# Optimization experiments

Measured on AMD Instinct MI355X. Metric: run time of the kernel, lower is better.

The kernel has to match this reference:

```python
import jax, jax.numpy as jnp
import numpy as np

HEADS = 16
DIM_HEAD = 64
LN_EPS = 1e-3  # keras LayerNormalization default


def setup_inputs() -> dict:
    key = jax.random.key(0)
    ks = jax.random.split(key, 4)
    B, N, D = 8, 512, 1024
    inner = HEADS * DIM_HEAD  # 1024
    return {
        "x": jax.random.normal(ks[0], (B, N, D), dtype=jnp.float32),
        "w_qkv": jax.random.normal(ks[1], (D, 3 * inner), dtype=jnp.float32) * (D ** -0.5),
        "reattn_w": jax.random.normal(ks[2], (HEADS, HEADS), dtype=jnp.float32),
        "ln_gamma": jnp.ones((HEADS,), dtype=jnp.float32),
        "ln_beta": jnp.zeros((HEADS,), dtype=jnp.float32),
        "w_out": jax.random.normal(ks[3], (inner, D), dtype=jnp.float32) * (inner ** -0.5),
        "b_out": jnp.zeros((D,), dtype=jnp.float32),
    }


def reference(x, w_qkv, reattn_w, ln_gamma, ln_beta, w_out, b_out):
    B, N, D = x.shape
    H, dh = HEADS, DIM_HEAD
    scale = dh ** -0.5

    qkv = x @ w_qkv  # [B, N, 3*H*dh]
    q, k, v = jnp.split(qkv, 3, axis=-1)
    # b n (h d) -> b h n d
    to_heads = lambda t: t.reshape(B, N, H, dh).transpose(0, 2, 1, 3)
    q, k, v = to_heads(q), to_heads(k), to_heads(v)

    dots = jnp.einsum("bhid,bhjd->bhij", q, k) * scale  # [B, H, N, N]
    attn = jax.nn.softmax(dots, axis=-1)

    # re-attention: mix across heads
    attn = jnp.einsum("bhij,hg->bgij", attn, reattn_w)

    # LayerNorm over the head axis (axis=1), keras default eps
    mean = jnp.mean(attn, axis=1, keepdims=True)
    var = jnp.var(attn, axis=1, keepdims=True)
    attn = (attn - mean) * jax.lax.rsqrt(var + LN_EPS)
    attn = attn * ln_gamma[None, :, None, None] + ln_beta[None, :, None, None]

    out = jnp.einsum("bhij,bhjd->bhid", attn, v)  # [B, H, N, dh]
    out = out.transpose(0, 2, 1, 3).reshape(B, N, H * dh)  # b h n d -> b n (h d)
    return out @ w_out + b_out
```

## Files before the change

### kernel.cpp

```cpp
#include <hip/hip_runtime.h>
#include <math.h>

#define BB 8
#define NN 512
#define DD 1024
#define HH 16
#define DH 64
#define INNER 1024
#define QKV3 3072
#define PSTR (NN * NN + 64)

typedef __attribute__((ext_vector_type(8))) short short8;
typedef __attribute__((ext_vector_type(4))) float f32x4;

#define AS1 __attribute__((address_space(1)))
#define AS3 __attribute__((address_space(3)))

__device__ __forceinline__ float4 ld4(const float* p) { return *(const float4*)p; }

__device__ __forceinline__ unsigned short f2bf(float f) {
    unsigned u = __float_as_uint(f);
    return (unsigned short)((u + 0x7fffu + ((u >> 16) & 1u)) >> 16);
}
__device__ __forceinline__ float bf2f(unsigned short u) {
    return __uint_as_float(((unsigned)u) << 16);
}

__global__ void conv_bf16(const float* __restrict__ in, unsigned short* __restrict__ out) {
    size_t i = ((size_t)blockIdx.x * 256 + threadIdx.x) * 4;
    float4 v = ld4(in + i);
    ushort4 o;
    o.x = f2bf(v.x); o.y = f2bf(v.y); o.z = f2bf(v.z); o.w = f2bf(v.w);
    *(ushort4*)(out + i) = o;
}

__global__ void convT_bf16(const float* __restrict__ in, unsigned short* __restrict__ out,
                           int K, int N) {
    __shared__ float t[32][33];
    const int n0 = blockIdx.x * 32, k0 = blockIdx.y * 32;
    const int tx = threadIdx.x & 31, ty = threadIdx.x >> 5;
#pragma unroll
    for (int l = 0; l < 4; ++l)
        t[ty + 8 * l][tx] = in[(size_t)(k0 + ty + 8 * l) * N + n0 + tx];
    __syncthreads();
#pragma unroll
    for (int l = 0; l < 4; ++l)
        out[(size_t)(n0 + ty + 8 * l) * K + k0 + tx] = f2bf(t[tx][ty + 8 * l]);
}

__global__ __launch_bounds__(256) void gemm_bf16(
    const unsigned short* __restrict__ A, const unsigned short* __restrict__ Bt,
    float* __restrict__ C, const float* __restrict__ bias, int M, int N, int K) {
    __shared__ short As[128 * 32];
    __shared__ short Bs[128 * 32];
    const int tid = threadIdx.x;
    const int w = tid >> 6, l = tid & 63;
    const int bm = blockIdx.y * 128, bn = blockIdx.x * 128;
    const int wm = (w >> 1) * 64, wn = (w & 1) * 64;
    const int lrow = l & 15, lq = l >> 4;

    f32x4 acc[4][4];
#pragma unroll
    for (int i = 0; i < 4; ++i)
#pragma unroll
        for (int j = 0; j < 4; ++j) acc[i][j] = (f32x4){0.f, 0.f, 0.f, 0.f};

    for (int k0 = 0; k0 < K; k0 += 32) {
#pragma unroll
        for (int t = 0; t < 2; ++t) {
            const int q = w * 2 + t;
            const int li = q * 512 + l * 8;
            const int row = li >> 5, kc = li & 31;
            const unsigned short* ga = A + (size_t)(bm + row) * K + k0 + kc;
            __builtin_amdgcn_global_load_lds(
                (const AS1 void*)ga, (AS3 void*)(As + q * 512), 16, 0, 0);
            const unsigned short* gb = Bt + (size_t)(bn + row) * K + k0 + kc;
            __builtin_amdgcn_global_load_lds(
                (const AS1 void*)gb, (AS3 void*)(Bs + q * 512), 16, 0, 0);
        }
        __syncthreads();

        short8 a[4], b[4];
#pragma unroll
        for (int i = 0; i < 4; ++i)
            a[i] = *(const short8*)(As + (wm + i * 16 + lrow) * 32 + lq * 8);
#pragma unroll
        for (int j = 0; j < 4; ++j)
            b[j] = *(const short8*)(Bs + (wn + j * 16 + lrow) * 32 + lq * 8);
#pragma unroll
        for (int i = 0; i < 4; ++i)
#pragma unroll
            for (int j = 0; j < 4; ++j)
                acc[i][j] = __builtin_amdgcn_mfma_f32_16x16x32_bf16(a[i], b[j], acc[i][j], 0, 0, 0);
        __syncthreads();
    }

#pragma unroll
    for (int i = 0; i < 4; ++i)
#pragma unroll
        for (int j = 0; j < 4; ++j) {
            const int col = bn + wn + j * 16 + lrow;
            const float bv = bias ? bias[col] : 0.f;
#pragma unroll
            for (int r = 0; r < 4; ++r) {
                const int row = bm + wm + i * 16 + lq * 4 + r;
                C[(size_t)row * N + col] = acc[i][j][r] + bv;
            }
        }
}

__device__ __forceinline__ void stage_st(const unsigned short* __restrict__ G, int K,
                                         int row0, int kt, short* dst_half,
                                         int w, int l) {
    const int grow = row0 + w * 16 + (l >> 2);
    const int gcol = kt * 32 + (((l & 3) * 8) ^ ((l & 32) ? 16 : 0));
    __builtin_amdgcn_global_load_lds(
        (const AS1 void*)(G + (size_t)grow * K + gcol),
        (AS3 void*)(dst_half + w * 512), 16, 0, 0);
}

__global__ __launch_bounds__(512, 2) void gemm256_bf(
    const unsigned short* __restrict__ A, const unsigned short* __restrict__ Bt,
    unsigned short* __restrict__ C, int M, int N, int K) {
    __shared__ __align__(16) short lds_[2 * 16384];
    const int tid = threadIdx.x;
    const int w = tid >> 6, l = tid & 63;
    const int wm = w >> 2, wn = w & 3;
    const int lrow = l & 15, lq = l >> 4;
    const int bm = blockIdx.y * 256, bn = blockIdx.x * 256;
    const int NT = K >> 5;

    const int aoff = lrow * 32 + ((lq * 8) ^ ((lrow & 8) ? 16 : 0));
    const int bsub = (wn & 1) * 4;

    f32x4 acc[8][4];
#pragma unroll
    for (int i = 0; i < 8; ++i)
#pragma unroll
        for (int j = 0; j < 4; ++j) acc[i][j] = (f32x4){0.f, 0.f, 0.f, 0.f};

    stage_st(A,  K, bm,       0, lds_ + 0,     w, l);
    stage_st(A,  K, bm + 128, 0, lds_ + 4096,  w, l);
    stage_st(Bt, K, bn,       0, lds_ + 8192,  w, l);
    stage_st(Bt, K, bn + 128, 0, lds_ + 12288, w, l);
    asm volatile("s_waitcnt vmcnt(0)" ::: "memory");
    __builtin_amdgcn_s_barrier();

    for (int t = 0; t < NT; ++t) {
        const int s = t & 1;
        if (t + 1 < NT) {
            short* nb = lds_ + (s ^ 1) * 16384;
            stage_st(A,  K, bm,       t + 1, nb,         w, l);
            stage_st(A,  K, bm + 128, t + 1, nb + 4096,  w, l);
            stage_st(Bt, K, bn,       t + 1, nb + 8192,  w, l);
            stage_st(Bt, K, bn + 128, t + 1, nb + 12288, w, l);
        }
        const short* Ah = lds_ + s * 16384 + wm * 4096;
        const short* Bh = lds_ + s * 16384 + 8192 + (wn >> 1) * 4096;
        short8 a[8], bfr[4];
#pragma unroll
        for (int i = 0; i < 8; ++i)
            a[i] = *(const short8*)(Ah + i * 512 + aoff);
#pragma unroll
        for (int j = 0; j < 4; ++j)
            bfr[j] = *(const short8*)(Bh + (bsub + j) * 512 + aoff);

        asm volatile("s_waitcnt lgkmcnt(0)" ::: "memory");
        __builtin_amdgcn_sched_barrier(0);

        __builtin_amdgcn_s_setprio(1);
#pragma unroll
        for (int i = 0; i < 8; ++i)
#pragma unroll
            for (int j = 0; j < 4; ++j)
                acc[i][j] = __builtin_amdgcn_mfma_f32_16x16x32_bf16(a[i], bfr[j], acc[i][j], 0, 0, 0);
        __builtin_amdgcn_s_setprio(0);

        asm volatile("s_waitcnt vmcnt(0)" ::: "memory");
        __builtin_amdgcn_s_barrier();
    }

#pragma unroll
    for (int fr = 0; fr < 8; ++fr)
#pragma unroll
        for (int fc = 0; fc < 4; ++fc) {
            const int col = bn + wn * 64 + fc * 16 + lrow;
#pragma unroll
            for (int r = 0; r < 4; ++r) {
                const int row = bm + wm * 128 + fr * 16 + lq * 4 + r;
                C[(size_t)row * N + col] = f2bf(acc[fr][fc][r]);
            }
        }
}

__global__ __launch_bounds__(256) void scores_stream(
    const unsigned short* __restrict__ qkvb, unsigned short* __restrict__ attnb,
    float* __restrict__ lsum2) {
    __shared__ unsigned short Ks[256 * 64];
    __shared__ unsigned short obuf[4][16][68];
    const int bh = blockIdx.x;
    const int h = bh & 15, b = bh >> 4;
    const int jh = blockIdx.y;
    const int w = threadIdx.x >> 6, l = threadIdx.x & 63;
    const int i0 = blockIdx.z * 64 + w * 16;
    const int lrow = l & 15, lq = l >> 4;

    const unsigned short* kbase =
        qkvb + (size_t)(b * NN + jh * 256) * QKV3 + INNER + h * DH;
#pragma unroll
    for (int i = 0; i < 8; ++i) {
        const int r = (w * 8 + i) * 8 + (l >> 3);
        const int c = (l & 7) ^ (r & 7);
        __builtin_amdgcn_global_load_lds(
            (const AS1 void*)(kbase + (size_t)r * QKV3 + c * 8),
            (AS3 void*)(Ks + (w * 8 + i) * 512), 16, 0, 0);
    }

    const unsigned short* qb = qkvb + (size_t)(b * NN) * QKV3 + h * DH + lq * 8;
    const short8 qf0 = *(const short8*)(qb + (size_t)(i0 + lrow) * QKV3);
    const short8 qf1 = *(const short8*)(qb + (size_t)(i0 + lrow) * QKV3 + 32);

    asm volatile("s_waitcnt vmcnt(0)" ::: "memory");
    __syncthreads();

    unsigned short* obase = attnb + (size_t)bh * PSTR + (size_t)i0 * NN + jh * 256;
    const int sw = lrow & 7;
    float lacc = 0.f;
#pragma unroll
    for (int jt = 0; jt < 16; ++jt) {
        const int R = jt * 16 + lrow;
        const short8 kf0 = *(const short8*)(Ks + R * 64 + ((lq ^ sw) * 8));
        const short8 kf1 = *(const short8*)(Ks + R * 64 + (((4 + lq) ^ sw) * 8));
        f32x4 acc = (f32x4){0.f, 0.f, 0.f, 0.f};
        acc = __builtin_amdgcn_mfma_f32_16x16x32_bf16(kf0, qf0, acc, 0, 0, 0);
        acc = __builtin_amdgcn_mfma_f32_16x16x32_bf16(kf1, qf1, acc, 0, 0, 0);
        float e0 = __expf(acc[0] * 0.125f);
        float e1 = __expf(acc[1] * 0.125f);
        float e2 = __expf(acc[2] * 0.125f);
        float e3 = __expf(acc[3] * 0.125f);
        lacc += (e0 + e1) + (e2 + e3);
        ushort4 o;
        o.x = f2bf(e0); o.y = f2bf(e1); o.z = f2bf(e2); o.w = f2bf(e3);
        *(ushort4*)(&obuf[w][lrow][(jt & 3) * 16 + lq * 4]) = o;
        if ((jt & 3) == 3) {
            const int jb = (jt >> 2) * 64;
#pragma unroll
            for (int q = 0; q < 4; ++q) {
                const int rr = q * 4 + (l >> 4);
                const int cc = l & 15;
                *(ushort4*)(obase + (size_t)rr * NN + jb + cc * 4) =
                    *(const ushort4*)(&obuf[w][rr][cc * 4]);
            }
        }
    }
    lacc += __shfl_xor(lacc, 16, 64);
    lacc += __shfl_xor(lacc, 32, 64);
    if (lq == 0)
        lsum2[(size_t)jh * BB * HH * NN + (size_t)bh * NN + i0 + lrow] = lacc;
}

__global__ void reattn_ln_bf(unsigned short* __restrict__ attnb,
                             const float* __restrict__ lsum2,
                             const float* __restrict__ rw,
                             const float* __restrict__ gamma,
                             const float* __restrict__ beta) {
    __shared__ float w[16][16];
    __shared__ float gs[16], bs[16];
    const int tid = threadIdx.x;
    ((float*)w)[tid] = rw[tid];
    if (tid < 16) { gs[tid] = gamma[tid]; bs[tid] = beta[tid]; }
    __syncthreads();

    const size_t idx = (size_t)blockIdx.x * 256 + tid;
    const int j4 = (int)(idx & 127);
    const int i = (int)((idx >> 7) & 511);
    const int b = (int)(idx >> 16);
    unsigned short* base = attnb + (size_t)(b * HH) * PSTR + (size_t)i * NN + j4 * 4;
    const float* l0 = lsum2 + (size_t)(b * HH) * NN + i;
    const float* l1 = l0 + (size_t)BB * HH * NN;

    float v[16][4];
#pragma unroll
    for (int h = 0; h < 16; ++h) {
        const float linv = 1.0f / (l0[h * NN] + l1[h * NN]);
        ushort4 u = *(const ushort4*)(base + (size_t)h * PSTR);
        v[h][0] = bf2f(u.x) * linv; v[h][1] = bf2f(u.y) * linv;
        v[h][2] = bf2f(u.z) * linv; v[h][3] = bf2f(u.w) * linv;
    }
    float o[16][4];
    float me[4] = {0.f, 0.f, 0.f, 0.f};
#pragma unroll
    for (int g = 0; g < 16; ++g) {
        float s0 = 0.f, s1 = 0.f, s2 = 0.f, s3 = 0.f;
#pragma unroll
        for (int h = 0; h < 16; ++h) {
            const float wg = w[h][g];
            s0 += v[h][0] * wg; s1 += v[h][1] * wg;
            s2 += v[h][2] * wg; s3 += v[h][3] * wg;
        }
        o[g][0] = s0; o[g][1] = s1; o[g][2] = s2; o[g][3] = s3;
        me[0] += s0; me[1] += s1; me[2] += s2; me[3] += s3;
    }
#pragma unroll
    for (int r = 0; r < 4; ++r) me[r] *= 0.0625f;
    float va[4] = {0.f, 0.f, 0.f, 0.f};
#pragma unroll
    for (int g = 0; g < 16; ++g)
#pragma unroll
        for (int r = 0; r < 4; ++r) {
            float d = o[g][r] - me[r];
            va[r] += d * d;
        }
    float ri[4];
#pragma unroll
    for (int r = 0; r < 4; ++r) ri[r] = rsqrtf(va[r] * 0.0625f + 1e-3f);
#pragma unroll
    for (int g = 0; g < 16; ++g) {
        ushort4 u;
        u.x = f2bf((o[g][0] - me[0]) * ri[0] * gs[g] + bs[g]);
        u.y = f2bf((o[g][1] - me[1]) * ri[1] * gs[g] + bs[g]);
        u.z = f2bf((o[g][2] - me[2]) * ri[2] * gs[g] + bs[g]);
        u.w = f2bf((o[g][3] - me[3]) * ri[3] * gs[g] + bs[g]);
        *(ushort4*)(base + (size_t)g * PSTR) = u;
    }
}

__global__ void transpose_v(const unsigned short* __restrict__ qkvb,
                            unsigned short* __restrict__ vT) {
    __shared__ unsigned short t[32][33];
    const int bh = blockIdx.z;
    const int h = bh & 15, b = bh >> 4;
    const int j0 = blockIdx.x * 32, d0 = blockIdx.y * 32;
    const int tx = threadIdx.x & 31, ty = threadIdx.x >> 5;
    const unsigned short* src = qkvb + (size_t)(b * NN) * QKV3 + 2 * INNER + h * DH;
#pragma unroll
    for (int k = 0; k < 4; ++k)
        t[ty + 8 * k][tx] = src[(size_t)(j0 + ty + 8 * k) * QKV3 + d0 + tx];
    __syncthreads();
    unsigned short* dst = vT + (size_t)bh * DH * NN;
#pragma unroll
    for (int k = 0; k < 4; ++k)
        dst[(size_t)(d0 + ty + 8 * k) * NN + j0 + tx] = t[tx][ty + 8 * k];
}

__global__ __launch_bounds__(256) void pv_mfma(
    const unsigned short* __restrict__ attnb, const unsigned short* __restrict__ vT,
    unsigned short* __restrict__ outhb) {
    const int bh = blockIdx.x;
    const int h = bh & 15, b = bh >> 4;
    const int i0 = blockIdx.y * 128;
    __shared__ short Ps[128 * 64];
    __shared__ short Vs[64 * 64];
    const int tid = threadIdx.x;
    const int w = tid >> 6, l = tid & 63;
    const int lrow = l & 15, lq = l >> 4;
    const int lr8 = l >> 3;
    const int swd = ((l & 7) ^ (lr8 & 7)) * 8;

    f32x4 acc[2][4];
#pragma unroll
    for (int ic = 0; ic < 2; ++ic)
#pragma unroll
        for (int dt = 0; dt < 4; ++dt) acc[ic][dt] = (f32x4){0.f, 0.f, 0.f, 0.f};

    const unsigned short* pb = attnb + (size_t)bh * PSTR + (size_t)i0 * NN;
    const unsigned short* vb = vT + (size_t)bh * DH * NN;

    for (int j0 = 0; j0 < NN; j0 += 64) {
#pragma unroll
        for (int t = 0; t < 4; ++t) {
            int c = w * 4 + t;
            int r = c * 8 + lr8;
            __builtin_amdgcn_global_load_lds(
                (const AS1 void*)(pb + (size_t)r * NN + j0 + swd),
                (AS3 void*)(Ps + c * 512), 16, 0, 0);
        }
#pragma unroll
        for (int t = 0; t < 2; ++t) {
            int c = w * 2 + t;
            int d = c * 8 + lr8;
            __builtin_amdgcn_global_load_lds(
                (const AS1 void*)(vb + (size_t)d * NN + j0 + swd),
                (AS3 void*)(Vs + c * 512), 16, 0, 0);
        }
        __syncthreads();

#pragma unroll
        for (int kh = 0; kh < 2; ++kh) {
            short8 vf[4];
#pragma unroll
            for (int dt = 0; dt < 4; ++dt)
                vf[dt] = *(const short8*)(Vs + (dt * 16 + lrow) * 64 + (((kh * 4 + lq) ^ (lrow & 7)) * 8));
#pragma unroll
            for (int ic = 0; ic < 2; ++ic) {
                short8 pf = *(const short8*)(Ps + (w * 32 + ic * 16 + lrow) * 64 + (((kh * 4 + lq) ^ (lrow & 7)) * 8));
#pragma unroll
                for (int dt = 0; dt < 4; ++dt)
                    acc[ic][dt] = __builtin_amdgcn_mfma_f32_16x16x32_bf16(vf[dt], pf, acc[ic][dt], 0, 0, 0);
            }
        }
        __syncthreads();
    }

#pragma unroll
    for (int ic = 0; ic < 2; ++ic) {
        unsigned short* orow = outhb +
            ((size_t)(b * NN + i0 + w * 32 + ic * 16 + lrow)) * INNER + h * DH + lq * 4;
#pragma unroll
        for (int dt = 0; dt < 4; ++dt) {
            ushort4 o;
            o.x = f2bf(acc[ic][dt][0]); o.y = f2bf(acc[ic][dt][1]);
            o.z = f2bf(acc[ic][dt][2]); o.w = f2bf(acc[ic][dt][3]);
            *(ushort4*)(orow + dt * 16) = o;
        }
    }
}

extern "C" void kernel_launch(void* const* d_in, const int* in_sizes, int n_in,
                              void* d_out, int out_size, void* d_ws, size_t ws_size,
                              hipStream_t stream) {
    const float* x        = (const float*)d_in[0];
    const float* w_qkv    = (const float*)d_in[1];
    const float* reattn_w = (const float*)d_in[2];
    const float* ln_gamma = (const float*)d_in[3];
    const float* ln_beta  = (const float*)d_in[4];
    const float* w_out    = (const float*)d_in[5];
    const float* b_out    = (const float*)d_in[6];
    float* out = (float*)d_out;

    unsigned short* qkvb  = (unsigned short*)d_ws;
    unsigned short* attnb = qkvb + (size_t)BB * NN * QKV3;
    unsigned short* vTb   = attnb + (size_t)BB * HH * PSTR;
    unsigned short* outhb = vTb + (size_t)BB * HH * DH * NN;
    unsigned short* xb    = outhb + (size_t)BB * NN * INNER;
    unsigned short* wqkvT = xb + (size_t)BB * NN * DD;
    unsigned short* woutT = wqkvT + (size_t)DD * QKV3;
    float*          lsum2 = (float*)(woutT + (size_t)INNER * INNER);

    dim3 blk(256);

    conv_bf16<<<dim3((BB * NN * DD) / 1024), blk, 0, stream>>>(x, xb);
    convT_bf16<<<dim3(QKV3 / 32, DD / 32), blk, 0, stream>>>(w_qkv, wqkvT, DD, QKV3);
    convT_bf16<<<dim3(INNER / 32, INNER / 32), blk, 0, stream>>>(w_out, woutT, INNER, INNER);

    gemm256_bf<<<dim3(QKV3 / 256, (BB * NN) / 256), dim3(512), 0, stream>>>(
        xb, wqkvT, qkvb, BB * NN, QKV3, DD);

    scores_stream<<<dim3(BB * HH, 2, NN / 64), blk, 0, stream>>>(qkvb, attnb, lsum2);

    reattn_ln_bf<<<dim3((BB * NN * NN) / 1024), blk, 0, stream>>>(
        attnb, lsum2, reattn_w, ln_gamma, ln_beta);

    transpose_v<<<dim3(NN / 32, DH / 32, BB * HH), blk, 0, stream>>>(qkvb, vTb);

    pv_mfma<<<dim3(BB * HH, NN / 128), blk, 0, stream>>>(attnb, vTb, outhb);

    gemm_bf16<<<dim3(INNER / 128, (BB * NN) / 128), blk, 0, stream>>>(
        outhb, woutT, out, b_out, BB * NN, INNER, INNER);
}
```

Before: 219.2 us.

## Double-buffer LDS in output GEMM and PV kernels, fuse conversion launches

```diff
diff --git a/kernel.cpp b/kernel.cpp
--- a/kernel.cpp
+++ b/kernel.cpp
@@ -26,19 +26,31 @@
     return __uint_as_float(((unsigned)u) << 16);
 }
 
-__global__ void conv_bf16(const float* __restrict__ in, unsigned short* __restrict__ out) {
-    size_t i = ((size_t)blockIdx.x * 256 + threadIdx.x) * 4;
-    float4 v = ld4(in + i);
-    ushort4 o;
-    o.x = f2bf(v.x); o.y = f2bf(v.y); o.z = f2bf(v.z); o.w = f2bf(v.w);
-    *(ushort4*)(out + i) = o;
-}
-
-__global__ void convT_bf16(const float* __restrict__ in, unsigned short* __restrict__ out,
-                           int K, int N) {
+__global__ void preprocess(const float* __restrict__ x, unsigned short* __restrict__ xb,
+                           const float* __restrict__ wq, unsigned short* __restrict__ wqT,
+                           const float* __restrict__ wo, unsigned short* __restrict__ woT) {
     __shared__ float t[32][33];
-    const int n0 = blockIdx.x * 32, k0 = blockIdx.y * 32;
-    const int tx = threadIdx.x & 31, ty = threadIdx.x >> 5;
+    const int tid = threadIdx.x;
+    const int bx = blockIdx.x;
+    if (bx < 4096) {
+        size_t i = ((size_t)bx * 256 + tid) * 4;
+        float4 v = ld4(x + i);
+        ushort4 o;
+        o.x = f2bf(v.x); o.y = f2bf(v.y); o.z = f2bf(v.z); o.w = f2bf(v.w);
+        *(ushort4*)(xb + i) = o;
+        return;
+    }
+    const float* in; unsigned short* out; int K, N, n0, k0;
+    if (bx < 7168) {
+        const int bb = bx - 4096;
+        in = wq; out = wqT; K = DD; N = QKV3;
+        n0 = (bb % 96) * 32; k0 = (bb / 96) * 32;
+    } else {
+        const int bb = bx - 7168;
+        in = wo; out = woT; K = INNER; N = INNER;
+        n0 = (bb & 31) * 32; k0 = (bb >> 5) * 32;
+    }
+    const int tx = tid & 31, ty = tid >> 5;
 #pragma unroll
     for (int l = 0; l < 4; ++l)
         t[ty + 8 * l][tx] = in[(size_t)(k0 + ty + 8 * l) * N + n0 + tx];
@@ -48,16 +60,34 @@
         out[(size_t)(n0 + ty + 8 * l) * K + k0 + tx] = f2bf(t[tx][ty + 8 * l]);
 }
 
+__device__ __forceinline__ void stage128(const unsigned short* __restrict__ A,
+                                         const unsigned short* __restrict__ Bt,
+                                         int K, int bm, int bn, int kt,
+                                         short* sb, int w, int l) {
+#pragma unroll
+    for (int t = 0; t < 2; ++t) {
+        const int q = w * 2 + t;
+        const int li = q * 512 + l * 8;
+        const int row = li >> 5, kc = li & 31;
+        __builtin_amdgcn_global_load_lds(
+            (const AS1 void*)(A + (size_t)(bm + row) * K + kt * 32 + kc),
+            (AS3 void*)(sb + q * 512), 16, 0, 0);
+        __builtin_amdgcn_global_load_lds(
+            (const AS1 void*)(Bt + (size_t)(bn + row) * K + kt * 32 + kc),
+            (AS3 void*)(sb + 4096 + q * 512), 16, 0, 0);
+    }
+}
+
 __global__ __launch_bounds__(256) void gemm_bf16(
     const unsigned short* __restrict__ A, const unsigned short* __restrict__ Bt,
     float* __restrict__ C, const float* __restrict__ bias, int M, int N, int K) {
-    __shared__ short As[128 * 32];
-    __shared__ short Bs[128 * 32];
+    __shared__ __align__(16) short lds_[2 * 8192];
     const int tid = threadIdx.x;
     const int w = tid >> 6, l = tid & 63;
     const int bm = blockIdx.y * 128, bn = blockIdx.x * 128;
     const int wm = (w >> 1) * 64, wn = (w & 1) * 64;
     const int lrow = l & 15, lq = l >> 4;
+    const int NT = K >> 5;
 
     f32x4 acc[4][4];
 #pragma unroll
@@ -65,34 +95,37 @@
 #pragma unroll
         for (int j = 0; j < 4; ++j) acc[i][j] = (f32x4){0.f, 0.f, 0.f, 0.f};
 
-    for (int k0 = 0; k0 < K; k0 += 32) {
-#pragma unroll
-        for (int t = 0; t < 2; ++t) {
-            const int q = w * 2 + t;
-            const int li = q * 512 + l * 8;
-            const int row = li >> 5, kc = li & 31;
-            const unsigned short* ga = A + (size_t)(bm + row) * K + k0 + kc;
-            __builtin_amdgcn_global_load_lds(
-                (const AS1 void*)ga, (AS3 void*)(As + q * 512), 16, 0, 0);
-            const unsigned short* gb = Bt + (size_t)(bn + row) * K + k0 + kc;
-            __builtin_amdgcn_global_load_lds(
-                (const AS1 void*)gb, (AS3 void*)(Bs + q * 512), 16, 0, 0);
-        }
-        __syncthreads();
-
+    stage128(A, Bt, K, bm, bn, 0, lds_, w, l);
+    asm volatile("s_waitcnt vmcnt(0)" ::: "memory");
+    __builtin_amdgcn_s_barrier();
+
+    for (int t = 0; t < NT; ++t) {
+        const int s = t & 1;
+        if (t + 1 < NT)
+            stage128(A, Bt, K, bm, bn, t + 1, lds_ + (s ^ 1) * 8192, w, l);
+        const short* As_ = lds_ + s * 8192;
+        const short* Bs_ = As_ + 4096;
         short8 a[4], b[4];
 #pragma unroll
         for (int i = 0; i < 4; ++i)
-            a[i] = *(const short8*)(As + (wm + i * 16 + lrow) * 32 + lq * 8);
+            a[i] = *(const short8*)(As_ + (wm + i * 16 + lrow) * 32 + lq * 8);
 #pragma unroll
         for (int j = 0; j < 4; ++j)
-            b[j] = *(const short8*)(Bs + (wn + j * 16 + lrow) * 32 + lq * 8);
+            b[j] = *(const short8*)(Bs_ + (wn + j * 16 + lrow) * 32 + lq * 8);
+
+        asm volatile("s_waitcnt lgkmcnt(0)" ::: "memory");
+        __builtin_amdgcn_sched_barrier(0);
+
+        __builtin_amdgcn_s_setprio(1);
 #pragma unroll
         for (int i = 0; i < 4; ++i)
 #pragma unroll
             for (int j = 0; j < 4; ++j)
                 acc[i][j] = __builtin_amdgcn_mfma_f32_16x16x32_bf16(a[i], b[j], acc[i][j], 0, 0, 0);
-        __syncthreads();
+        __builtin_amdgcn_s_setprio(0);
+
+        asm volatile("s_waitcnt vmcnt(0)" ::: "memory");
+        __builtin_amdgcn_s_barrier();
     }
 
 #pragma unroll
@@ -343,14 +376,36 @@
         dst[(size_t)(d0 + ty + 8 * k) * NN + j0 + tx] = t[tx][ty + 8 * k];
 }
 
+__device__ __forceinline__ void stage_pv(const unsigned short* __restrict__ pb,
+                                         const unsigned short* __restrict__ vb,
+                                         int j0, short* Ps, short* Vs,
+                                         int w, int l, int lr8, int swd) {
+#pragma unroll
+    for (int t = 0; t < 4; ++t) {
+        int c = w * 4 + t;
+        int r = c * 8 + lr8;
+        __builtin_amdgcn_global_load_lds(
+            (const AS1 void*)(pb + (size_t)r * NN + j0 + swd),
+            (AS3 void*)(Ps + c * 512), 16, 0, 0);
+    }
+#pragma unroll
+    for (int t = 0; t < 2; ++t) {
+        int c = w * 2 + t;
+        int d = c * 8 + lr8;
+        __builtin_amdgcn_global_load_lds(
+            (const AS1 void*)(vb + (size_t)d * NN + j0 + swd),
+            (AS3 void*)(Vs + c * 512), 16, 0, 0);
+    }
+}
+
 __global__ __launch_bounds__(256) void pv_mfma(
     const unsigned short* __restrict__ attnb, const unsigned short* __restrict__ vT,
     unsigned short* __restrict__ outhb) {
     const int bh = blockIdx.x;
     const int h = bh & 15, b = bh >> 4;
     const int i0 = blockIdx.y * 128;
-    __shared__ short Ps[128 * 64];
-    __shared__ short Vs[64 * 64];
+    __shared__ __align__(16) short Ps[2][128 * 64];
+    __shared__ __align__(16) short Vs[2][64 * 64];
     const int tid = threadIdx.x;
     const int w = tid >> 6, l = tid & 63;
     const int lrow = l & 15, lq = l >> 4;
@@ -366,40 +421,44 @@
     const unsigned short* pb = attnb + (size_t)bh * PSTR + (size_t)i0 * NN;
     const unsigned short* vb = vT + (size_t)bh * DH * NN;
 
-    for (int j0 = 0; j0 < NN; j0 += 64) {
-#pragma unroll
-        for (int t = 0; t < 4; ++t) {
-            int c = w * 4 + t;
-            int r = c * 8 + lr8;
-            __builtin_amdgcn_global_load_lds(
-                (const AS1 void*)(pb + (size_t)r * NN + j0 + swd),
-                (AS3 void*)(Ps + c * 512), 16, 0, 0);
-        }
-#pragma unroll
-        for (int t = 0; t < 2; ++t) {
-            int c = w * 2 + t;
-            int d = c * 8 + lr8;
-            __builtin_amdgcn_global_load_lds(
-                (const AS1 void*)(vb + (size_t)d * NN + j0 + swd),
-                (AS3 void*)(Vs + c * 512), 16, 0, 0);
-        }
-        __syncthreads();
-
+    stage_pv(pb, vb, 0, Ps[0], Vs[0], w, l, lr8, swd);
+    asm volatile("s_waitcnt vmcnt(0)" ::: "memory");
+    __builtin_amdgcn_s_barrier();
+
+    for (int js = 0; js < 8; ++js) {
+        const int s = js & 1;
+        if (js + 1 < 8)
+            stage_pv(pb, vb, (js + 1) * 64, Ps[s ^ 1], Vs[s ^ 1], w, l, lr8, swd);
+
+        short8 vf[8], pf[4];
 #pragma unroll
         for (int kh = 0; kh < 2; ++kh) {
-            short8 vf[4];
 #pragma unroll
             for (int dt = 0; dt < 4; ++dt)
-                vf[dt] = *(const short8*)(Vs + (dt * 16 + lrow) * 64 + (((kh * 4 + lq) ^ (lrow & 7)) * 8));
-#pragma unroll
-            for (int ic = 0; ic < 2; ++ic) {
-                short8 pf = *(const short8*)(Ps + (w * 32 + ic * 16 + lrow) * 64 + (((kh * 4 + lq) ^ (lrow & 7)) * 8));
+                vf[kh * 4 + dt] = *(const short8*)(
+                    &Vs[s][(dt * 16 + lrow) * 64 + (((kh * 4 + lq) ^ (lrow & 7)) * 8)]);
+#pragma unroll
+            for (int ic = 0; ic < 2; ++ic)
+                pf[kh * 2 + ic] = *(const short8*)(
+                    &Ps[s][(w * 32 + ic * 16 + lrow) * 64 + (((kh * 4 + lq) ^ (lrow & 7)) * 8)]);
+        }
+
+        asm volatile("s_waitcnt lgkmcnt(0)" ::: "memory");
+        __builtin_amdgcn_sched_barrier(0);
+
+        __builtin_amdgcn_s_setprio(1);
+#pragma unroll
+        for (int kh = 0; kh < 2; ++kh)
+#pragma unroll
+            for (int ic = 0; ic < 2; ++ic)
 #pragma unroll
                 for (int dt = 0; dt < 4; ++dt)
-                    acc[ic][dt] = __builtin_amdgcn_mfma_f32_16x16x32_bf16(vf[dt], pf, acc[ic][dt], 0, 0, 0);
-            }
-        }
-        __syncthreads();
+                    acc[ic][dt] = __builtin_amdgcn_mfma_f32_16x16x32_bf16(
+                        vf[kh * 4 + dt], pf[kh * 2 + ic], acc[ic][dt], 0, 0, 0);
+        __builtin_amdgcn_s_setprio(0);
+
+        asm volatile("s_waitcnt vmcnt(0)" ::: "memory");
+        __builtin_amdgcn_s_barrier();
     }
 
 #pragma unroll
@@ -439,9 +498,7 @@
 
     dim3 blk(256);
 
-    conv_bf16<<<dim3((BB * NN * DD) / 1024), blk, 0, stream>>>(x, xb);
-    convT_bf16<<<dim3(QKV3 / 32, DD / 32), blk, 0, stream>>>(w_qkv, wqkvT, DD, QKV3);
-    convT_bf16<<<dim3(INNER / 32, INNER / 32), blk, 0, stream>>>(w_out, woutT, INNER, INNER);
+    preprocess<<<dim3(8192), blk, 0, stream>>>(x, xb, w_qkv, wqkvT, w_out, woutT);
 
     gemm256_bf<<<dim3(QKV3 / 256, (BB * NN) / 256), dim3(512), 0, stream>>>(
         xb, wqkvT, qkvb, BB * NN, QKV3, DD);
```

Result: faster. 208.4 us (-4.9%).
